# Performance work log

Measured on AMD Instinct MI355X. Metric: run time of the kernel, lower is better.

The kernel has to match this reference:

```python
import jax, jax.numpy as jnp
import numpy as np

B, S, D_IN, H, D_HEAD = 4, 2048, 768, 12, 64


def setup_inputs() -> dict:
    key = jax.random.key(0)
    kx, kq, kk, kv, kc = jax.random.split(key, 5)
    x = jax.random.normal(kx, (B, S, D_IN), dtype=jnp.float32)
    # torch.rand -> uniform [0,1)
    wq = jax.random.uniform(kq, (H, D_IN, D_HEAD), dtype=jnp.float32)
    wk = jax.random.uniform(kk, (H, D_IN, D_HEAD), dtype=jnp.float32)
    wv = jax.random.uniform(kv, (H, D_IN, D_HEAD), dtype=jnp.float32)
    wc = jax.random.uniform(kc, (D_HEAD, H * D_HEAD), dtype=jnp.float32)
    return {"x": x, "wq": wq, "wk": wk, "wv": wv, "wc": wc}


def reference(x, wq, wk, wv, wc):
    # per-head projections: weight [H, D_in, D_head], x [B, S, D_in] -> [B, H, S, D_head]
    q = jnp.einsum('hkd,bsk->bhsd', wq, x)
    k = jnp.einsum('hkd,bsk->bhsd', wk, x)
    v = jnp.einsum('hkd,bsk->bhsd', wv, x)
    scale = jnp.sqrt(jnp.float32(D_HEAD))
    scores = jax.nn.softmax(jnp.einsum('bhld,bhnd->bhln', q, k) / scale, axis=-1)
    z = jnp.einsum('bhln,bhnd->bhld', scores, v)        # [B, H, S, D_head]
    z = jnp.transpose(z, (0, 2, 1, 3)).reshape(B, S, H * D_HEAD)
    # output projection: wc [D_head, H*D_head] -> [B, S, D_head]
    return jnp.einsum('ij,bsj->bsi', wc, z)
```

## Files before the change

### kernel.cpp

```cpp
#include <hip/hip_runtime.h>
#include <hip/hip_bf16.h>
#include <math.h>

#define BB 4
#define SS 2048
#define DIN 768
#define HH 12
#define DH 64
#define NT (SS / 64)

typedef __attribute__((ext_vector_type(8))) _Float16 f16x8;
typedef __attribute__((ext_vector_type(4))) _Float16 f16x4;
typedef __attribute__((ext_vector_type(2))) _Float16 f16x2;
typedef __attribute__((ext_vector_type(4))) float f32x4;
typedef __attribute__((ext_vector_type(16))) float f32x16;
typedef __attribute__((ext_vector_type(4))) unsigned u32x4;

__device__ inline void splith(float v, _Float16& hi, _Float16& lo) {
    hi = (_Float16)v;
    lo = (_Float16)(v - (float)hi);
}
__device__ inline unsigned packh2(float a, float b) {
    f16x2 h; h[0] = (_Float16)a; h[1] = (_Float16)b;
    return __builtin_bit_cast(unsigned, h);
}
__device__ inline f16x8 ldb64x2(const _Float16* p) {
    const uint2* q = reinterpret_cast<const uint2*>(p);
    uint2 a = q[0], b = q[1];
    u32x4 u = {a.x, a.y, b.x, b.y};
    return __builtin_bit_cast(f16x8, u);
}
__device__ inline void stb64x2(_Float16* p, uint4 v) {
    uint2* q = reinterpret_cast<uint2*>(p);
    q[0] = make_uint2(v.x, v.y);
    q[1] = make_uint2(v.z, v.w);
}
__device__ inline f32x16 zero16() {
    f32x16 v;
    #pragma unroll
    for (int i = 0; i < 16; ++i) v[i] = 0.f;
    return v;
}

__global__ __launch_bounds__(256) void prep_w_kernel(
    const float* __restrict__ wq, const float* __restrict__ wk, const float* __restrict__ wv,
    _Float16* __restrict__ whi, _Float16* __restrict__ wlo)
{
    const int kt = blockIdx.x, h = blockIdx.y, which = blockIdx.z;
    const float* w = (which == 0) ? wq : (which == 1) ? wk : wv;
    w += (size_t)h * (DIN * DH);
    const size_t plane = ((size_t)which * HH + h) * (size_t)(64 * DIN);

    __shared__ float tile[64][65];
    const int t = threadIdx.x;
    {
        int r = t >> 2, n0 = (t & 3) * 16;
        const float* src = w + (size_t)(kt * 64 + r) * DH + n0;
        #pragma unroll
        for (int q = 0; q < 4; ++q) {
            float4 v = *reinterpret_cast<const float4*>(src + q * 4);
            tile[r][n0 + q * 4 + 0] = v.x; tile[r][n0 + q * 4 + 1] = v.y;
            tile[r][n0 + q * 4 + 2] = v.z; tile[r][n0 + q * 4 + 3] = v.w;
        }
    }
    __syncthreads();
    {
        int n = t >> 2, k0 = (t & 3) * 16;
        f16x8 h0, h1, l0, l1;
        #pragma unroll
        for (int j = 0; j < 8; ++j) {
            _Float16 hh, ll;
            splith(tile[k0 + j][n], hh, ll);     h0[j] = hh; l0[j] = ll;
            splith(tile[k0 + 8 + j][n], hh, ll); h1[j] = hh; l1[j] = ll;
        }
        size_t base = plane + (size_t)n * DIN + kt * 64 + k0;
        *reinterpret_cast<f16x8*>(whi + base)     = h0;
        *reinterpret_cast<f16x8*>(whi + base + 8) = h1;
        *reinterpret_cast<f16x8*>(wlo + base)     = l0;
        *reinterpret_cast<f16x8*>(wlo + base + 8) = l1;
    }
}

__global__ __launch_bounds__(256) void prep_wc_kernel(
    const float* __restrict__ wc,
    _Float16* __restrict__ wch, _Float16* __restrict__ wcl)
{
    int idx = (blockIdx.x * 256 + threadIdx.x) * 8;
    float4 a = *reinterpret_cast<const float4*>(wc + idx);
    float4 b = *reinterpret_cast<const float4*>(wc + idx + 4);
    float f[8] = {a.x, a.y, a.z, a.w, b.x, b.y, b.z, b.w};
    f16x8 hv, lv;
    #pragma unroll
    for (int j = 0; j < 8; ++j) {
        _Float16 hh, ll;
        splith(f[j], hh, ll);
        hv[j] = hh; lv[j] = ll;
    }
    *reinterpret_cast<f16x8*>(wch + idx) = hv;
    *reinterpret_cast<f16x8*>(wcl + idx) = lv;
}

__global__ __launch_bounds__(256) void qkv_proj_kernel(
    const float* __restrict__ x,
    const _Float16* __restrict__ whi, const _Float16* __restrict__ wlo,
    _Float16* __restrict__ qh, _Float16* __restrict__ ql,
    _Float16* __restrict__ kh, _Float16* __restrict__ kl,
    _Float16* __restrict__ vt)
{
    const int flat = blockIdx.x;
    const int xcd  = flat & 7;
    const int rest = flat >> 3;
    const int mt   = xcd * 16 + (rest & 15);
    const int hw   = rest >> 4;
    const int which = hw / HH, h = hw % HH;
    const int m0 = mt * 64;
    const size_t wplane = ((size_t)which * HH + h) * (size_t)(64 * DIN);

    __shared__ _Float16 xsh[64][40], xsl[64][40], wsh[64][40], wsl[64][40];
    __shared__ _Float16 vtile[64][72];

    const int t = threadIdx.x;
    const int lane = t & 63, wid = t >> 6;
    const int fr = lane & 15, fg = lane >> 4, g8 = fg * 8;

    f32x4 acc[4];
    #pragma unroll
    for (int n = 0; n < 4; ++n) acc[n] = (f32x4){0.f, 0.f, 0.f, 0.f};

    for (int ks = 0; ks < DIN / 32; ++ks) {
        const int k0 = ks * 32;
        {
            int r = t >> 2, c8 = (t & 3) * 8;
            const float* xp = x + (size_t)(m0 + r) * DIN + k0 + c8;
            float4 a = *reinterpret_cast<const float4*>(xp);
            float4 b = *reinterpret_cast<const float4*>(xp + 4);
            float f[8] = {a.x, a.y, a.z, a.w, b.x, b.y, b.z, b.w};
            f16x8 xh, xl;
            #pragma unroll
            for (int j = 0; j < 8; ++j) {
                _Float16 hh, ll;
                splith(f[j], hh, ll);
                xh[j] = hh; xl[j] = ll;
            }
            *reinterpret_cast<f16x8*>(&xsh[r][c8]) = xh;
            *reinterpret_cast<f16x8*>(&xsl[r][c8]) = xl;
            size_t wb = wplane + (size_t)r * DIN + k0 + c8;
            *reinterpret_cast<f16x8*>(&wsh[r][c8]) = *reinterpret_cast<const f16x8*>(whi + wb);
            *reinterpret_cast<f16x8*>(&wsl[r][c8]) = *reinterpret_cast<const f16x8*>(wlo + wb);
        }
        __syncthreads();
        f16x8 ah = *reinterpret_cast<const f16x8*>(&xsh[wid * 16 + fr][g8]);
        f16x8 al = *reinterpret_cast<const f16x8*>(&xsl[wid * 16 + fr][g8]);
        #pragma unroll
        for (int n = 0; n < 4; ++n) {
            f16x8 bh = *reinterpret_cast<const f16x8*>(&wsh[n * 16 + fr][g8]);
            f16x8 bl = *reinterpret_cast<const f16x8*>(&wsl[n * 16 + fr][g8]);
            acc[n] = __builtin_amdgcn_mfma_f32_16x16x32_f16(ah, bh, acc[n], 0, 0, 0);
            acc[n] = __builtin_amdgcn_mfma_f32_16x16x32_f16(ah, bl, acc[n], 0, 0, 0);
            acc[n] = __builtin_amdgcn_mfma_f32_16x16x32_f16(al, bh, acc[n], 0, 0, 0);
        }
        __syncthreads();
    }

    if (which == 2) {
        #pragma unroll
        for (int n = 0; n < 4; ++n)
            #pragma unroll
            for (int j = 0; j < 4; ++j)
                vtile[n * 16 + fr][wid * 16 + fg * 4 + j] = (_Float16)acc[n][j];
        __syncthreads();
        int r = t >> 2, c0 = (t & 3) * 16;
        int b0 = m0 >> 11, s0 = m0 & 2047;
        size_t base = (((size_t)b0 * HH + h) * DH + r) * SS + s0 + c0;
        *reinterpret_cast<uint4*>(vt + base)     = *reinterpret_cast<uint4*>(&vtile[r][c0]);
        *reinterpret_cast<uint4*>(vt + base + 8) = *reinterpret_cast<uint4*>(&vtile[r][c0 + 8]);
    } else {
        #pragma unroll
        for (int n = 0; n < 4; ++n)
            #pragma unroll
            for (int j = 0; j < 4; ++j) {
                int row = wid * 16 + fg * 4 + j;
                int m = m0 + row, bb = m >> 11, ss = m & 2047;
                size_t idx = (((size_t)bb * HH + h) * SS + ss) * DH + n * 16 + fr;
                float val = acc[n][j];
                if (which == 0) val *= 0.125f;
                _Float16 hi, lo;
                splith(val, hi, lo);
                if (which == 0) { qh[idx] = hi; ql[idx] = lo; }
                else            { kh[idx] = hi; kl[idx] = lo; }
            }
    }
}

__global__ __launch_bounds__(256, 3) void attn_kernel(
    const _Float16* __restrict__ qhp, const _Float16* __restrict__ qlp,
    const _Float16* __restrict__ khp, const _Float16* __restrict__ klp,
    const _Float16* __restrict__ vtp,
    _Float16* __restrict__ z)
{
    const int flat = blockIdx.x;
    const int remap = (flat & 7) * 96 + (flat >> 3);
    const int qt = remap & 15;
    const int h  = (remap >> 4) % HH;
    const int b  = remap / (16 * HH);

    const size_t headbase = ((size_t)b * HH + h) * (size_t)(SS * DH);
    const _Float16* Qh = qhp + headbase;
    const _Float16* Ql = qlp + headbase;
    const _Float16* Kh = khp + headbase;
    const _Float16* Kl = klp + headbase;
    const _Float16* Vt = vtp + headbase;

    __shared__ _Float16 ksh[64][68], ksl[64][68], vts[64][68];

    const int t = threadIdx.x;
    const int lane = t & 63, w = t >> 6;
    const int qcol = lane & 31, hi = lane >> 5;
    const int r4 = t >> 2, c16 = (t & 3) * 16;

    const size_t qbase = (size_t)(qt * 128 + w * 32 + qcol) * DH + hi * 8;
    f16x8 bqh[4], bql[4];
    #pragma unroll
    for (int ks = 0; ks < 4; ++ks) {
        bqh[ks] = *reinterpret_cast<const f16x8*>(Qh + qbase + 16 * ks);
        bql[ks] = *reinterpret_cast<const f16x8*>(Ql + qbase + 16 * ks);
    }

    uint4 rk0, rk1, rl0, rl1, rv0, rv1;
    auto prefetch = [&](int kt) {
        size_t sk = (size_t)(kt * 64 + r4) * DH + c16;
        rk0 = *reinterpret_cast<const uint4*>(Kh + sk);
        rk1 = *reinterpret_cast<const uint4*>(Kh + sk + 8);
        rl0 = *reinterpret_cast<const uint4*>(Kl + sk);
        rl1 = *reinterpret_cast<const uint4*>(Kl + sk + 8);
        size_t sv = (size_t)r4 * SS + kt * 64 + c16;
        rv0 = *reinterpret_cast<const uint4*>(Vt + sv);
        rv1 = *reinterpret_cast<const uint4*>(Vt + sv + 8);
    };
    prefetch(0);

    float mrun = -INFINITY, lrun = 0.f;
    f32x16 oc0 = zero16(), oc1 = zero16();

    for (int kt = 0; kt < NT; ++kt) {
        __syncthreads();
        stb64x2(&ksh[r4][c16],     rk0);
        stb64x2(&ksh[r4][c16 + 8], rk1);
        stb64x2(&ksl[r4][c16],     rl0);
        stb64x2(&ksl[r4][c16 + 8], rl1);
        stb64x2(&vts[r4][c16],     rv0);
        stb64x2(&vts[r4][c16 + 8], rv1);
        if (kt + 1 < NT) prefetch(kt + 1);
        __syncthreads();

        f32x16 c0 = zero16(), c1 = zero16();
        #pragma unroll
        for (int ks = 0; ks < 4; ++ks) {
            const int doff = hi * 8 + 16 * ks;
            f16x8 a0h = ldb64x2(&ksh[qcol][doff]);
            f16x8 a0l = ldb64x2(&ksl[qcol][doff]);
            c0 = __builtin_amdgcn_mfma_f32_32x32x16_f16(a0h, bqh[ks], c0, 0, 0, 0);
            c0 = __builtin_amdgcn_mfma_f32_32x32x16_f16(a0h, bql[ks], c0, 0, 0, 0);
            c0 = __builtin_amdgcn_mfma_f32_32x32x16_f16(a0l, bqh[ks], c0, 0, 0, 0);
            f16x8 a1h = ldb64x2(&ksh[qcol + 32][doff]);
            f16x8 a1l = ldb64x2(&ksl[qcol + 32][doff]);
            c1 = __builtin_amdgcn_mfma_f32_32x32x16_f16(a1h, bqh[ks], c1, 0, 0, 0);
            c1 = __builtin_amdgcn_mfma_f32_32x32x16_f16(a1h, bql[ks], c1, 0, 0, 0);
            c1 = __builtin_amdgcn_mfma_f32_32x32x16_f16(a1l, bqh[ks], c1, 0, 0, 0);
        }

        float mx = c0[0];
        #pragma unroll
        for (int i = 1; i < 16; ++i) mx = fmaxf(mx, c0[i]);
        #pragma unroll
        for (int i = 0; i < 16; ++i) mx = fmaxf(mx, c1[i]);
        mx = fmaxf(mx, __shfl_xor(mx, 32));
        float nm = fmaxf(mrun, mx);
        float corr = __expf(mrun - nm);
        float sum = 0.f;
        #pragma unroll
        for (int i = 0; i < 16; ++i) { float p = __expf(c0[i] - nm); c0[i] = p; sum += p; }
        #pragma unroll
        for (int i = 0; i < 16; ++i) { float p = __expf(c1[i] - nm); c1[i] = p; sum += p; }
        sum += __shfl_xor(sum, 32);
        lrun = lrun * corr + sum;
        mrun = nm;
        #pragma unroll
        for (int i = 0; i < 16; ++i) { oc0[i] *= corr; oc1[i] *= corr; }

        auto mk = [](float s0, float s1, float s2, float s3,
                     float s4, float s5, float s6, float s7) -> f16x8 {
            unsigned a0 = packh2(s0, s1), a1 = packh2(s2, s3);
            unsigned b0 = packh2(s4, s5), b1 = packh2(s6, s7);
            asm volatile("v_permlane32_swap_b32 %0, %1" : "+v"(a0), "+v"(b0));
            asm volatile("v_permlane32_swap_b32 %0, %1" : "+v"(a1), "+v"(b1));
            u32x4 u = {a0, a1, b0, b1};
            return __builtin_bit_cast(f16x8, u);
        };
        f16x8 bp0 = mk(c0[0], c0[1], c0[2],  c0[3],  c0[4],  c0[5],  c0[6],  c0[7]);
        f16x8 bp1 = mk(c0[8], c0[9], c0[10], c0[11], c0[12], c0[13], c0[14], c0[15]);
        f16x8 bp2 = mk(c1[0], c1[1], c1[2],  c1[3],  c1[4],  c1[5],  c1[6],  c1[7]);
        f16x8 bp3 = mk(c1[8], c1[9], c1[10], c1[11], c1[12], c1[13], c1[14], c1[15]);

        {
            const int k0 = hi * 8;
            f16x8 av;
            av = ldb64x2(&vts[qcol][k0]);            oc0 = __builtin_amdgcn_mfma_f32_32x32x16_f16(av, bp0, oc0, 0, 0, 0);
            av = ldb64x2(&vts[qcol + 32][k0]);       oc1 = __builtin_amdgcn_mfma_f32_32x32x16_f16(av, bp0, oc1, 0, 0, 0);
            av = ldb64x2(&vts[qcol][k0 + 16]);       oc0 = __builtin_amdgcn_mfma_f32_32x32x16_f16(av, bp1, oc0, 0, 0, 0);
            av = ldb64x2(&vts[qcol + 32][k0 + 16]);  oc1 = __builtin_amdgcn_mfma_f32_32x32x16_f16(av, bp1, oc1, 0, 0, 0);
            av = ldb64x2(&vts[qcol][k0 + 32]);       oc0 = __builtin_amdgcn_mfma_f32_32x32x16_f16(av, bp2, oc0, 0, 0, 0);
            av = ldb64x2(&vts[qcol + 32][k0 + 32]);  oc1 = __builtin_amdgcn_mfma_f32_32x32x16_f16(av, bp2, oc1, 0, 0, 0);
            av = ldb64x2(&vts[qcol][k0 + 48]);       oc0 = __builtin_amdgcn_mfma_f32_32x32x16_f16(av, bp3, oc0, 0, 0, 0);
            av = ldb64x2(&vts[qcol + 32][k0 + 48]);  oc1 = __builtin_amdgcn_mfma_f32_32x32x16_f16(av, bp3, oc1, 0, 0, 0);
        }
    }

    float inv = 1.0f / lrun;
    size_t zb = ((size_t)b * SS + qt * 128 + w * 32 + qcol) * (size_t)(HH * DH) + h * DH;
    #pragma unroll
    for (int g = 0; g < 4; ++g) {
        f16x4 v0, v1;
        #pragma unroll
        for (int i = 0; i < 4; ++i) {
            v0[i] = (_Float16)(oc0[4 * g + i] * inv);
            v1[i] = (_Float16)(oc1[4 * g + i] * inv);
        }
        *reinterpret_cast<f16x4*>(z + zb + 8 * g + 4 * hi)      = v0;
        *reinterpret_cast<f16x4*>(z + zb + 32 + 8 * g + 4 * hi) = v1;
    }
}

__global__ __launch_bounds__(256) void outproj_kernel(
    const _Float16* __restrict__ z,
    const _Float16* __restrict__ wch, const _Float16* __restrict__ wcl,
    float* __restrict__ out)
{
    const int mt = blockIdx.x, m0 = mt * 64;
    __shared__ _Float16 zs[64][40], wh_[64][40], wl_[64][40];

    const int t = threadIdx.x;
    const int lane = t & 63, wid = t >> 6;
    const int fr = lane & 15, fg = lane >> 4, g8 = fg * 8;

    f32x4 acc[4];
    #pragma unroll
    for (int n = 0; n < 4; ++n) acc[n] = (f32x4){0.f, 0.f, 0.f, 0.f};

    for (int ks = 0; ks < DIN / 32; ++ks) {
        const int k0 = ks * 32;
        {
            int r = t >> 2, c8 = (t & 3) * 8;
            *reinterpret_cast<f16x8*>(&zs[r][c8]) =
                *reinterpret_cast<const f16x8*>(z + (size_t)(m0 + r) * DIN + k0 + c8);
            size_t wb = (size_t)r * DIN + k0 + c8;
            *reinterpret_cast<f16x8*>(&wh_[r][c8]) = *reinterpret_cast<const f16x8*>(wch + wb);
            *reinterpret_cast<f16x8*>(&wl_[r][c8]) = *reinterpret_cast<const f16x8*>(wcl + wb);
        }
        __syncthreads();
        f16x8 az = *reinterpret_cast<const f16x8*>(&zs[wid * 16 + fr][g8]);
        #pragma unroll
        for (int n = 0; n < 4; ++n) {
            f16x8 bh = *reinterpret_cast<const f16x8*>(&wh_[n * 16 + fr][g8]);
            f16x8 bl = *reinterpret_cast<const f16x8*>(&wl_[n * 16 + fr][g8]);
            acc[n] = __builtin_amdgcn_mfma_f32_16x16x32_f16(az, bh, acc[n], 0, 0, 0);
            acc[n] = __builtin_amdgcn_mfma_f32_16x16x32_f16(az, bl, acc[n], 0, 0, 0);
        }
        __syncthreads();
    }

    #pragma unroll
    for (int n = 0; n < 4; ++n)
        #pragma unroll
        for (int j = 0; j < 4; ++j) {
            int row = m0 + wid * 16 + fg * 4 + j;
            out[(size_t)row * DH + n * 16 + fr] = acc[n][j];
        }
}

extern "C" void kernel_launch(void* const* d_in, const int* in_sizes, int n_in,
                              void* d_out, int out_size, void* d_ws, size_t ws_size,
                              hipStream_t stream) {
    const float* x  = (const float*)d_in[0];
    const float* wq = (const float*)d_in[1];
    const float* wk = (const float*)d_in[2];
    const float* wv = (const float*)d_in[3];
    const float* wc = (const float*)d_in[4];
    float* out = (float*)d_out;

    const size_t wpl   = (size_t)3 * HH * 64 * DIN;
    const size_t plane = (size_t)BB * HH * SS * DH;
    _Float16* whi = (_Float16*)d_ws;
    _Float16* wlo = whi + wpl;
    _Float16* wch = wlo + wpl;
    _Float16* wcl = wch + (size_t)64 * DIN;
    _Float16* qh  = wcl + (size_t)64 * DIN;
    _Float16* ql  = qh + plane;
    _Float16* kh  = ql + plane;
    _Float16* kl  = kh + plane;
    _Float16* vt  = kl + plane;
    _Float16* zz  = vt + plane;

    prep_w_kernel<<<dim3(12, HH, 3), 256, 0, stream>>>(wq, wk, wv, whi, wlo);
    prep_wc_kernel<<<24, 256, 0, stream>>>(wc, wch, wcl);
    qkv_proj_kernel<<<4608, 256, 0, stream>>>(x, whi, wlo, qh, ql, kh, kl, vt);
    attn_kernel<<<768, 256, 0, stream>>>(qh, ql, kh, kl, vt, zz);
    outproj_kernel<<<128, 256, 0, stream>>>(zz, wch, wcl, out);
}
```

Baseline: 258.7 us.

## Fuse Q/K/V projections per block and prefetch next k-slice into registers

Each qkv_proj block now computes all three projections (Q, K, V) for one head and one row tile, so the x tile is loaded and split into hi/lo halves once instead of three times. The grid shrinks from 4608 to 1536 blocks. Global loads for the next k-step are issued into registers before the MFMA work of the current step, a register double-buffer that overlaps load latency with compute. In exchange the kernel uses three times the accumulators and more shared memory, which may lower occupancy.

```diff
diff --git a/kernel.cpp b/kernel.cpp
--- a/kernel.cpp
+++ b/kernel.cpp
@@ -111,30 +111,45 @@
     const int xcd  = flat & 7;
     const int rest = flat >> 3;
     const int mt   = xcd * 16 + (rest & 15);
-    const int hw   = rest >> 4;
-    const int which = hw / HH, h = hw % HH;
-    const int m0 = mt * 64;
-    const size_t wplane = ((size_t)which * HH + h) * (size_t)(64 * DIN);
-
-    __shared__ _Float16 xsh[64][40], xsl[64][40], wsh[64][40], wsl[64][40];
+    const int h    = rest >> 4;
+    const int m0   = mt * 64;
+
+    __shared__ _Float16 xsh[64][40], xsl[64][40];
+    __shared__ _Float16 wsh[3][64][40], wsl[3][64][40];
     __shared__ _Float16 vtile[64][72];
 
     const int t = threadIdx.x;
     const int lane = t & 63, wid = t >> 6;
     const int fr = lane & 15, fg = lane >> 4, g8 = fg * 8;
-
-    f32x4 acc[4];
-    #pragma unroll
-    for (int n = 0; n < 4; ++n) acc[n] = (f32x4){0.f, 0.f, 0.f, 0.f};
+    const int r = t >> 2, c8 = (t & 3) * 8;
+
+    f32x4 acc[3][4];
+    #pragma unroll
+    for (int p = 0; p < 3; ++p)
+        #pragma unroll
+        for (int n = 0; n < 4; ++n) acc[p][n] = (f32x4){0.f, 0.f, 0.f, 0.f};
+
+    float4 pxa, pxb;
+    uint4 pwh[3], pwl[3];
+    auto pre = [&](int ks) {
+        const int k0 = ks * 32;
+        const float* xp = x + (size_t)(m0 + r) * DIN + k0 + c8;
+        pxa = *reinterpret_cast<const float4*>(xp);
+        pxb = *reinterpret_cast<const float4*>(xp + 4);
+        const size_t wb = (size_t)r * DIN + k0 + c8;
+        #pragma unroll
+        for (int p = 0; p < 3; ++p) {
+            const size_t off = ((size_t)p * HH + h) * (size_t)(64 * DIN) + wb;
+            pwh[p] = *reinterpret_cast<const uint4*>(whi + off);
+            pwl[p] = *reinterpret_cast<const uint4*>(wlo + off);
+        }
+    };
+    pre(0);
 
     for (int ks = 0; ks < DIN / 32; ++ks) {
-        const int k0 = ks * 32;
+        __syncthreads();
         {
-            int r = t >> 2, c8 = (t & 3) * 8;
-            const float* xp = x + (size_t)(m0 + r) * DIN + k0 + c8;
-            float4 a = *reinterpret_cast<const float4*>(xp);
-            float4 b = *reinterpret_cast<const float4*>(xp + 4);
-            float f[8] = {a.x, a.y, a.z, a.w, b.x, b.y, b.z, b.w};
+            float f[8] = {pxa.x, pxa.y, pxa.z, pxa.w, pxb.x, pxb.y, pxb.z, pxb.w};
             f16x8 xh, xl;
             #pragma unroll
             for (int j = 0; j < 8; ++j) {
@@ -144,51 +159,50 @@
             }
             *reinterpret_cast<f16x8*>(&xsh[r][c8]) = xh;
             *reinterpret_cast<f16x8*>(&xsl[r][c8]) = xl;
-            size_t wb = wplane + (size_t)r * DIN + k0 + c8;
-            *reinterpret_cast<f16x8*>(&wsh[r][c8]) = *reinterpret_cast<const f16x8*>(whi + wb);
-            *reinterpret_cast<f16x8*>(&wsl[r][c8]) = *reinterpret_cast<const f16x8*>(wlo + wb);
-        }
-        __syncthreads();
+            #pragma unroll
+            for (int p = 0; p < 3; ++p) {
+                *reinterpret_cast<uint4*>(&wsh[p][r][c8]) = pwh[p];
+                *reinterpret_cast<uint4*>(&wsl[p][r][c8]) = pwl[p];
+            }
+        }
+        if (ks + 1 < DIN / 32) pre(ks + 1);
+        __syncthreads();
+
         f16x8 ah = *reinterpret_cast<const f16x8*>(&xsh[wid * 16 + fr][g8]);
         f16x8 al = *reinterpret_cast<const f16x8*>(&xsl[wid * 16 + fr][g8]);
         #pragma unroll
-        for (int n = 0; n < 4; ++n) {
-            f16x8 bh = *reinterpret_cast<const f16x8*>(&wsh[n * 16 + fr][g8]);
-            f16x8 bl = *reinterpret_cast<const f16x8*>(&wsl[n * 16 + fr][g8]);
-            acc[n] = __builtin_amdgcn_mfma_f32_16x16x32_f16(ah, bh, acc[n], 0, 0, 0);
-            acc[n] = __builtin_amdgcn_mfma_f32_16x16x32_f16(ah, bl, acc[n], 0, 0, 0);
-            acc[n] = __builtin_amdgcn_mfma_f32_16x16x32_f16(al, bh, acc[n], 0, 0, 0);
-        }
-        __syncthreads();
-    }
-
-    if (which == 2) {
-        #pragma unroll
-        for (int n = 0; n < 4; ++n)
+        for (int p = 0; p < 3; ++p)
             #pragma unroll
-            for (int j = 0; j < 4; ++j)
-                vtile[n * 16 + fr][wid * 16 + fg * 4 + j] = (_Float16)acc[n][j];
-        __syncthreads();
-        int r = t >> 2, c0 = (t & 3) * 16;
-        int b0 = m0 >> 11, s0 = m0 & 2047;
-        size_t base = (((size_t)b0 * HH + h) * DH + r) * SS + s0 + c0;
-        *reinterpret_cast<uint4*>(vt + base)     = *reinterpret_cast<uint4*>(&vtile[r][c0]);
-        *reinterpret_cast<uint4*>(vt + base + 8) = *reinterpret_cast<uint4*>(&vtile[r][c0 + 8]);
-    } else {
-        #pragma unroll
-        for (int n = 0; n < 4; ++n)
-            #pragma unroll
-            for (int j = 0; j < 4; ++j) {
-                int row = wid * 16 + fg * 4 + j;
-                int m = m0 + row, bb = m >> 11, ss = m & 2047;
-                size_t idx = (((size_t)bb * HH + h) * SS + ss) * DH + n * 16 + fr;
-                float val = acc[n][j];
-                if (which == 0) val *= 0.125f;
-                _Float16 hi, lo;
-                splith(val, hi, lo);
-                if (which == 0) { qh[idx] = hi; ql[idx] = lo; }
-                else            { kh[idx] = hi; kl[idx] = lo; }
+            for (int n = 0; n < 4; ++n) {
+                f16x8 bh = *reinterpret_cast<const f16x8*>(&wsh[p][n * 16 + fr][g8]);
+                f16x8 bl = *reinterpret_cast<const f16x8*>(&wsl[p][n * 16 + fr][g8]);
+                acc[p][n] = __builtin_amdgcn_mfma_f32_16x16x32_f16(ah, bh, acc[p][n], 0, 0, 0);
+                acc[p][n] = __builtin_amdgcn_mfma_f32_16x16x32_f16(ah, bl, acc[p][n], 0, 0, 0);
+                acc[p][n] = __builtin_amdgcn_mfma_f32_16x16x32_f16(al, bh, acc[p][n], 0, 0, 0);
             }
+    }
+
+    const int b0 = m0 >> 11, s0 = m0 & 2047;
+    #pragma unroll
+    for (int n = 0; n < 4; ++n)
+        #pragma unroll
+        for (int j = 0; j < 4; ++j) {
+            const int row = wid * 16 + fg * 4 + j;
+            const int ss = s0 + row;
+            const size_t idx = (((size_t)b0 * HH + h) * SS + ss) * DH + n * 16 + fr;
+            _Float16 hi, lo;
+            splith(acc[0][n][j] * 0.125f, hi, lo);
+            qh[idx] = hi; ql[idx] = lo;
+            splith(acc[1][n][j], hi, lo);
+            kh[idx] = hi; kl[idx] = lo;
+            vtile[n * 16 + fr][row] = (_Float16)acc[2][n][j];
+        }
+    __syncthreads();
+    {
+        int rr = t >> 2, c0 = (t & 3) * 16;
+        size_t base = (((size_t)b0 * HH + h) * DH + rr) * SS + s0 + c0;
+        *reinterpret_cast<uint4*>(vt + base)     = *reinterpret_cast<uint4*>(&vtile[rr][c0]);
+        *reinterpret_cast<uint4*>(vt + base + 8) = *reinterpret_cast<uint4*>(&vtile[rr][c0 + 8]);
     }
 }
 
@@ -403,7 +417,7 @@
 
     prep_w_kernel<<<dim3(12, HH, 3), 256, 0, stream>>>(wq, wk, wv, whi, wlo);
     prep_wc_kernel<<<24, 256, 0, stream>>>(wc, wch, wcl);
-    qkv_proj_kernel<<<4608, 256, 0, stream>>>(x, whi, wlo, qh, ql, kh, kl, vt);
+    qkv_proj_kernel<<<1536, 256, 0, stream>>>(x, whi, wlo, qh, ql, kh, kl, vt);
     attn_kernel<<<768, 256, 0, stream>>>(qh, ql, kh, kl, vt, zz);
     outproj_kernel<<<128, 256, 0, stream>>>(zz, wch, wcl, out);
 }
```

After: 382.2 us. 47.7% more time.
